# Kernel optimization log

Hardware: AMD Instinct MI355X
Metric: run time of the kernel (lower is better)

## Reference

```python
import jax, jax.numpy as jnp
import numpy as np

DIM = 1024
HEADS = 16
HEAD_DIM = DIM // HEADS
SCALE = HEAD_DIM ** -0.5


def setup_inputs() -> dict:
    key = jax.random.key(0)
    k_x, k_wqkv, k_bqkv, k_wp, k_bp = jax.random.split(key, 5)
    B, N, C = 8, 1024, DIM
    lim_qkv = 1.0 / np.sqrt(C)
    x = jax.random.normal(k_x, (B, N, C), dtype=jnp.float32)
    # store weights in [in, out] layout (torch Linear weight is [out,in]; y = x @ W.T + b)
    W_qkv = jax.random.uniform(k_wqkv, (C, 3 * C), dtype=jnp.float32, minval=-lim_qkv, maxval=lim_qkv)
    b_qkv = jax.random.uniform(k_bqkv, (3 * C,), dtype=jnp.float32, minval=-lim_qkv, maxval=lim_qkv)
    W_proj = jax.random.uniform(k_wp, (C, C), dtype=jnp.float32, minval=-lim_qkv, maxval=lim_qkv)
    b_proj = jax.random.uniform(k_bp, (C,), dtype=jnp.float32, minval=-lim_qkv, maxval=lim_qkv)
    return {"x": x, "W_qkv": W_qkv, "b_qkv": b_qkv, "W_proj": W_proj, "b_proj": b_proj}


def reference(x, W_qkv, b_qkv, W_proj, b_proj):
    B, N, C = x.shape
    H, D = HEADS, C // HEADS
    qkv = x @ W_qkv + b_qkv                          # [B, N, 3C]
    qkv = qkv.reshape(B, N, 3, H, D)
    q, k, v = jnp.moveaxis(qkv, 2, 0)                # each [B, N, H, D]
    q = q.transpose(0, 2, 1, 3)                      # [B, H, N, D]
    k = k.transpose(0, 2, 1, 3)
    v = v.transpose(0, 2, 1, 3)
    attn = jnp.einsum("bhnd,bhmd->bhnm", q, k) * SCALE
    attn = jax.nn.softmax(attn, axis=-1)
    out = jnp.einsum("bhnm,bhmd->bhnd", attn, v)     # [B, H, N, D]
    out = out.transpose(0, 2, 1, 3).reshape(B, N, C)
    return out @ W_proj + b_proj
```

## Files before the change

kernel.cpp:

```cpp
#include <hip/hip_runtime.h>
#include <hip/hip_bf16.h>


using bf16x8 = __attribute__((ext_vector_type(8))) short;
using f32x4  = __attribute__((ext_vector_type(4))) float;
using u16    = unsigned short;
using u16x8  = __attribute__((ext_vector_type(8))) unsigned short;
using u32x2  = __attribute__((ext_vector_type(2))) unsigned int;

__device__ __forceinline__ u16 f2bf(float f) {
  unsigned int u = __float_as_uint(f);
  u += 0x7FFFu + ((u >> 16) & 1u);
  return (u16)(u >> 16);
}
__device__ __forceinline__ float bf2f(u16 h) {
  return __uint_as_float(((unsigned int)h) << 16);
}
__device__ __forceinline__ unsigned cvt_pk_bf16(float a, float b) {
  unsigned r;
  asm("v_cvt_pk_bf16_f32 %0, %1, %2" : "=v"(r) : "v"(a), "v"(b));
  return r;
}
__device__ __forceinline__ float fexp2(float x) {
#if __has_builtin(__builtin_amdgcn_exp2f)
  return __builtin_amdgcn_exp2f(x);
#else
  return exp2f(x);
#endif
}

__device__ __forceinline__ void gload16(const u16* g, u16* lbase, int lane) {
#if __has_builtin(__builtin_amdgcn_global_load_lds)
  __builtin_amdgcn_global_load_lds(
      (const __attribute__((address_space(1))) void*)g,
      (__attribute__((address_space(3))) void*)lbase, 16, 0, 0);
#else
  *(u16x8*)(lbase + (size_t)lane * 8) = *(const u16x8*)g;
#endif
}

__device__ __forceinline__ void transpose_tile(
    const float* __restrict__ W, u16* __restrict__ Wt, int K, int N,
    int n0, int k0, float (*T)[65], int t)
{
  const int r = t >> 4, c4 = (t & 15) * 4;
  #pragma unroll
  for (int i = 0; i < 4; ++i) {
    f32x4 v = *(const f32x4*)&W[(size_t)(k0 + r + i * 16) * N + n0 + c4];
    T[r + i * 16][c4 + 0] = v.x;
    T[r + i * 16][c4 + 1] = v.y;
    T[r + i * 16][c4 + 2] = v.z;
    T[r + i * 16][c4 + 3] = v.w;
  }
  __syncthreads();
  const int nr = t >> 2, cs = (t & 3) * 16;
  u16x8 h0, h1;
  #pragma unroll
  for (int j = 0; j < 8; ++j) h0[j] = f2bf(T[cs + j][nr]);
  #pragma unroll
  for (int j = 0; j < 8; ++j) h1[j] = f2bf(T[cs + 8 + j][nr]);
  u16* dst = Wt + (size_t)(n0 + nr) * K + k0 + cs;
  *(u16x8*)dst = h0;
  *(u16x8*)(dst + 8) = h1;
}

__global__ __launch_bounds__(256) void prep(
    const float* __restrict__ x, u16* __restrict__ Xb,
    const float* __restrict__ Wq, u16* __restrict__ Wqt,
    const float* __restrict__ Wp, u16* __restrict__ Wpt)
{
  __shared__ float T[64][65];
  const int bid = blockIdx.x, t = threadIdx.x;
  if (bid < 4096) {
    size_t i = ((size_t)bid * 256 + t) * 8;
    f32x4 a = *(const f32x4*)(x + i);
    f32x4 b = *(const f32x4*)(x + i + 4);
    u16x8 h = { f2bf(a.x), f2bf(a.y), f2bf(a.z), f2bf(a.w),
                f2bf(b.x), f2bf(b.y), f2bf(b.z), f2bf(b.w) };
    *(u16x8*)(Xb + i) = h;
  } else if (bid < 4864) {
    const int tb = bid - 4096;
    transpose_tile(Wq, Wqt, 1024, 3072, (tb % 48) * 64, (tb / 48) * 64, T, t);
  } else {
    const int tb = bid - 4864;
    transpose_tile(Wp, Wpt, 1024, 1024, (tb % 16) * 64, (tb / 16) * 64, T, t);
  }
}

#define GEMM64_LOOP(ABASE, BBASE, AS, BS)                                     \
  const int tid = threadIdx.x;                                                \
  const int lane = tid & 63, wid = tid >> 6;                                  \
  const int wr = wid >> 1, wc = wid & 1;                                      \
  const int lg = lane >> 4, lc = lane & 15;                                   \
  const int row0 = blockIdx.x * 128, col0 = blockIdx.y * 128;                 \
  f32x4 acc[4][4];                                                            \
  _Pragma("unroll")                                                           \
  for (int m = 0; m < 4; ++m)                                                 \
    _Pragma("unroll")                                                         \
    for (int n = 0; n < 4; ++n) acc[m][n] = (f32x4){0.f, 0.f, 0.f, 0.f};      \
  const int srow = lane >> 3;                                       \
  const int sslot = (lane & 7) ^ srow;             \
  const u16* gA = (ABASE) + (size_t)(row0 + wid * 32 + srow) * 1024 + sslot * 8; \
  const u16* gB = (BBASE) + (size_t)(col0 + wid * 32 + srow) * 1024 + sslot * 8; \
  u16* lA = (AS) + wid * 2048;                                                \
  u16* lB = (BS) + wid * 2048;                                                \
  const int xr = lc & 7;                                                      \
  const int sl0 = ((0 + lg) ^ xr) * 8, sl1 = ((4 + lg) ^ xr) * 8;             \
  const int arow = (wr * 64 + lc) * 64, brow = (wc * 64 + lc) * 64;           \
  for (int k0 = 0; k0 < 1024; k0 += 64) {                                     \
    _Pragma("unroll")                                                         \
    for (int c = 0; c < 4; ++c) {                                             \
      gload16(gA + (size_t)c * 8192 + k0, lA + c * 512, lane);                \
      gload16(gB + (size_t)c * 8192 + k0, lB + c * 512, lane);                \
    }                                                                         \
    __syncthreads();                                                          \
    _Pragma("unroll")                                                         \
    for (int ks = 0; ks < 2; ++ks) {                                          \
      const int sl = ks ? sl1 : sl0;                                          \
      bf16x8 a[4], b[4];                                                      \
      _Pragma("unroll")                                                       \
      for (int m = 0; m < 4; ++m)                                             \
        a[m] = *(const bf16x8*)((AS) + arow + m * 1024 + sl);                 \
      _Pragma("unroll")                                                       \
      for (int n = 0; n < 4; ++n)                                             \
        b[n] = *(const bf16x8*)((BS) + brow + n * 1024 + sl);                 \
      __builtin_amdgcn_s_setprio(1);                                          \
      _Pragma("unroll")                                                       \
      for (int m = 0; m < 4; ++m)                                             \
        _Pragma("unroll")                                                     \
        for (int n = 0; n < 4; ++n)                                           \
          acc[m][n] = __builtin_amdgcn_mfma_f32_16x16x32_bf16(                \
              a[m], b[n], acc[m][n], 0, 0, 0);                                \
      __builtin_amdgcn_s_setprio(0);                                          \
    }                                                                         \
    __syncthreads();                                                          \
  }

__global__ __launch_bounds__(256, 2) void qkv_gemm2(
    const u16* __restrict__ Xb, const u16* __restrict__ Wt,
    const float* __restrict__ bias,
    u16* __restrict__ Qb, u16* __restrict__ Kb, u16* __restrict__ VtG)
{
  __shared__ __align__(16) u16 SM[128 * 130];
  u16* As = SM;
  u16* Bs = SM + 8192;
  u16* Tv = SM;

  GEMM64_LOOP(Xb, Wt, As, Bs)

  const int which = col0 >> 10;
  if (which == 2) {
    #pragma unroll
    for (int m = 0; m < 4; ++m) {
      #pragma unroll
      for (int n = 0; n < 4; ++n) {
        const int col = wc * 64 + n * 16 + lc;
        const float bv = bias[col0 + col];
        const int rrow = wr * 64 + m * 16 + lg * 4;
        #pragma unroll
        for (int r = 0; r < 4; ++r)
          Tv[(rrow + r) * 130 + col] = f2bf(acc[m][n][r] + bv);
      }
    }
    __syncthreads();
    const int c = tid >> 1, half = tid & 1;
    const int hh = c >> 6, d = c & 63;
    const int bb = row0 >> 10, nb = row0 & 1023;
    const int hbase = (col0 & 1023) >> 6;
    u16* vdst = VtG + ((size_t)(bb * 16 + hbase + hh) * 64 + d) * 1024
                + nb + half * 64;
    #pragma unroll
    for (int g = 0; g < 8; ++g) {
      u16x8 o;
      #pragma unroll
      for (int j = 0; j < 8; ++j)
        o[j] = Tv[(half * 64 + g * 8 + j) * 130 + c];
      *(u16x8*)(vdst + g * 8) = o;
    }
  } else {
    u16* dst = (which == 0) ? Qb : Kb;
    #pragma unroll
    for (int m = 0; m < 4; ++m) {
      #pragma unroll
      for (int n = 0; n < 4; ++n) {
        const int gc = col0 + wc * 64 + n * 16 + lc;
        const float bv = bias[gc];
        const int ci = gc & 1023, h = ci >> 6, d = ci & 63;
        const int gr0 = row0 + wr * 64 + m * 16 + lg * 4;
        const int bb = gr0 >> 10, nn0 = gr0 & 1023;
        #pragma unroll
        for (int r = 0; r < 4; ++r)
          dst[((size_t)(bb * 16 + h) * 1024 + nn0 + r) * 64 + d] =
              f2bf(acc[m][n][r] + bv);
      }
    }
  }
}

__global__ __launch_bounds__(256, 2) void attn_kernel(
    const u16* __restrict__ Q, const u16* __restrict__ K,
    const u16* __restrict__ Vt, u16* __restrict__ O)
{
  __shared__ __align__(16) u16 Ks[64 * 64];
  __shared__ __align__(16) u16 Vs[64 * 64];
  __shared__ __align__(16) u16 Pl[4 * 32 * 72];

  const int tid = threadIdx.x, lane = tid & 63, wid = tid >> 6;
  const int lg = lane >> 4, lc = lane & 15;
  const int bh = blockIdx.x;
  const int qt = blockIdx.y;
  const size_t base = (size_t)bh * 65536;
  const u16* Qp = Q + base;
  const u16* Kp = K + base;
  const u16* Vp = Vt + base;

  const float QSCALE = 0.125f * 1.44269504f;
  bf16x8 qf[2][2];
  #pragma unroll
  for (int f = 0; f < 2; ++f) {
    const u16* qsrc = Qp + (size_t)(qt * 128 + wid * 32 + f * 16 + lc) * 64 + lg * 8;
    #pragma unroll
    for (int ks = 0; ks < 2; ++ks) {
      u16x8 raw = *(const u16x8*)(qsrc + ks * 32);
      bf16x8 t;
      #pragma unroll
      for (int j = 0; j < 8; ++j) t[j] = (short)f2bf(bf2f(raw[j]) * QSCALE);
      qf[f][ks] = t;
    }
  }

  f32x4 o[2][4];
  #pragma unroll
  for (int f = 0; f < 2; ++f)
    #pragma unroll
    for (int d = 0; d < 4; ++d) o[f][d] = (f32x4){0.f, 0.f, 0.f, 0.f};
  float m_r[2] = {-1e30f, -1e30f};
  float l_r[2] = {0.f, 0.f};

  const int srow  = lane >> 3;
  const int sslot = (lane & 7) ^ srow;
  const u16* gK0 = Kp + (size_t)(wid * 16 + srow) * 64 + sslot * 8;
  const u16* gV0 = Vp + (size_t)(wid * 16 + srow) * 1024 + sslot * 8;
  u16* lK0 = Ks + wid * 1024;
  u16* lV0 = Vs + wid * 1024;

  const int xr = lc & 7;
  const int cof0 = ((0 + lg) ^ xr) * 8;
  const int cof1 = ((4 + lg) ^ xr) * 8;
  const int prow = (wid * 32 + lc) * 72;

  for (int kt = 0; kt < 16; ++kt) {
    gload16(gK0 + kt * 4096, lK0, lane);
    gload16(gK0 + kt * 4096 + 512, lK0 + 512, lane);
    gload16(gV0 + kt * 64, lV0, lane);
    gload16(gV0 + 8192 + kt * 64, lV0 + 512, lane);
    __syncthreads();

    f32x4 s[2][4];
    #pragma unroll
    for (int f = 0; f < 2; ++f)
      #pragma unroll
      for (int kb = 0; kb < 4; ++kb) s[f][kb] = (f32x4){0.f, 0.f, 0.f, 0.f};
    #pragma unroll
    for (int ks = 0; ks < 2; ++ks) {
      const int co = ks ? cof1 : cof0;
      #pragma unroll
      for (int kb = 0; kb < 4; ++kb) {
        bf16x8 kfr = *(const bf16x8*)(Ks + (kb * 16 + lc) * 64 + co);
        s[0][kb] = __builtin_amdgcn_mfma_f32_16x16x32_bf16(kfr, qf[0][ks], s[0][kb], 0, 0, 0);
        s[1][kb] = __builtin_amdgcn_mfma_f32_16x16x32_bf16(kfr, qf[1][ks], s[1][kb], 0, 0, 0);
      }
    }

    #pragma unroll
    for (int f = 0; f < 2; ++f) {
      f32x4 t01, t23;
      #pragma unroll
      for (int c = 0; c < 4; ++c) {
        t01[c] = fmaxf(s[f][0][c], s[f][1][c]);
        t23[c] = fmaxf(s[f][2][c], s[f][3][c]);
      }
      float t = fmaxf(fmaxf(fmaxf(t01[0], t01[1]), fmaxf(t01[2], t01[3])),
                      fmaxf(fmaxf(t23[0], t23[1]), fmaxf(t23[2], t23[3])));
      t = fmaxf(t, __shfl_xor(t, 16));
      t = fmaxf(t, __shfl_xor(t, 32));

      if (!__all((t - m_r[f]) <= 11.5f)) {
        float nm = fmaxf(m_r[f], t);
        float sc = fexp2(m_r[f] - nm);
        m_r[f] = nm;
        l_r[f] *= sc;
        #pragma unroll
        for (int r = 0; r < 4; ++r) {
          float scr = __shfl(sc, lg * 4 + r, 16);
          #pragma unroll
          for (int d = 0; d < 4; ++d) o[f][d][r] *= scr;
        }
      }

      float lsum = 0.f;
      #pragma unroll
      for (int kb = 0; kb < 4; ++kb) {
        f32x4 p;
        #pragma unroll
        for (int c = 0; c < 4; ++c) {
          p[c] = fexp2(s[f][kb][c] - m_r[f]);
          lsum += p[c];
        }
        u32x2 w = { cvt_pk_bf16(p[0], p[1]), cvt_pk_bf16(p[2], p[3]) };
        *(u32x2*)(Pl + prow + f * 1152 + kb * 16 + lg * 4) = w;
      }
      l_r[f] += lsum;
    }

    bf16x8 pa[2][2];
    #pragma unroll
    for (int f = 0; f < 2; ++f)
      #pragma unroll
      for (int ks = 0; ks < 2; ++ks)
        pa[f][ks] = *(const bf16x8*)(Pl + prow + f * 1152 + ks * 32 + lg * 8);
    #pragma unroll
    for (int d = 0; d < 4; ++d) {
      #pragma unroll
      for (int ks = 0; ks < 2; ++ks) {
        const int co = ks ? cof1 : cof0;
        bf16x8 vfr = *(const bf16x8*)(Vs + (d * 16 + lc) * 64 + co);
        o[0][d] = __builtin_amdgcn_mfma_f32_16x16x32_bf16(pa[0][ks], vfr, o[0][d], 0, 0, 0);
        o[1][d] = __builtin_amdgcn_mfma_f32_16x16x32_bf16(pa[1][ks], vfr, o[1][d], 0, 0, 0);
      }
    }
    __syncthreads();
  }

  const int b = bh >> 4, h = bh & 15;
  #pragma unroll
  for (int f = 0; f < 2; ++f) {
    float t = l_r[f];
    t += __shfl_xor(t, 16);
    t += __shfl_xor(t, 32);
    float linv = 1.0f / t;
    #pragma unroll
    for (int r = 0; r < 4; ++r) {
      float li = __shfl(linv, lg * 4 + r, 16);
      int n = qt * 128 + wid * 32 + f * 16 + lg * 4 + r;
      u16* dst = O + ((size_t)b * 1024 + n) * 1024 + h * 64 + lc;
      #pragma unroll
      for (int d = 0; d < 4; ++d) dst[d * 16] = f2bf(o[f][d][r] * li);
    }
  }
}

__global__ __launch_bounds__(256, 2) void proj_gemm2(
    const u16* __restrict__ Ab, const u16* __restrict__ Wt,
    const float* __restrict__ bias, float* __restrict__ Out)
{
  __shared__ __align__(16) u16 As[128 * 64];
  __shared__ __align__(16) u16 Bs[128 * 64];

  GEMM64_LOOP(Ab, Wt, As, Bs)

  #pragma unroll
  for (int m = 0; m < 4; ++m) {
    #pragma unroll
    for (int n = 0; n < 4; ++n) {
      #pragma unroll
      for (int r = 0; r < 4; ++r) {
        int gr = row0 + wr * 64 + m * 16 + lg * 4 + r;
        int gc = col0 + wc * 64 + n * 16 + lc;
        Out[(size_t)gr * 1024 + gc] = acc[m][n][r] + bias[gc];
      }
    }
  }
}

extern "C" void kernel_launch(void* const* d_in, const int* in_sizes, int n_in,
                              void* d_out, int out_size, void* d_ws, size_t ws_size,
                              hipStream_t stream) {
  const float* x     = (const float*)d_in[0];
  const float* W_qkv = (const float*)d_in[1];
  const float* b_qkv = (const float*)d_in[2];
  const float* W_prj = (const float*)d_in[3];
  const float* b_prj = (const float*)d_in[4];
  float* out = (float*)d_out;

  const size_t SEG = (size_t)8192 * 1024;
  char* ws = (char*)d_ws;
  u16* Xb  = (u16*)ws;
  u16* Ab  = Xb;
  u16* VtG = (u16*)(ws + SEG * 2);
  u16* Wqt = (u16*)(ws + SEG * 4);
  u16* Wpt = Wqt + (size_t)3072 * 1024;
  u16* Qb  = (u16*)d_out;
  u16* Kb  = Qb + SEG;

  prep<<<5120, 256, 0, stream>>>(x, Xb, W_qkv, Wqt, W_prj, Wpt);
  qkv_gemm2<<<dim3(64, 24), 256, 0, stream>>>(Xb, Wqt, b_qkv, Qb, Kb, VtG);
  attn_kernel<<<dim3(128, 8), 256, 0, stream>>>(Qb, Kb, VtG, Ab);
  proj_gemm2<<<dim3(64, 8), 256, 0, stream>>>(Ab, Wpt, b_prj, out);
}
```

Before: 150.0 us.

## Load K/V fragments directly from global into registers, drop LDS staging

The attention kernel no longer stages K and V tiles through shared memory with block-wide barriers. Each wave now loads its MFMA K and V fragments straight from global memory (relying on L1/L2 for reuse across the four waves), and the V loads are issued before the softmax so their latency overlaps it. Launch bounds are raised to allow four blocks per CU. The trade is redundant global/L2 traffic, since every wave fetches the full K/V tiles, plus higher register pressure under the tighter occupancy target, in exchange for removing the LDS round trip and the two __syncthreads per iteration.

```diff
diff --git a/kernel.cpp b/kernel.cpp
--- a/kernel.cpp
+++ b/kernel.cpp
@@ -197,12 +197,10 @@
   }
 }
 
-__global__ __launch_bounds__(256, 2) void attn_kernel(
+__global__ __launch_bounds__(256, 4) void attn_kernel(
     const u16* __restrict__ Q, const u16* __restrict__ K,
     const u16* __restrict__ Vt, u16* __restrict__ O)
 {
-  __shared__ __align__(16) u16 Ks[64 * 64];
-  __shared__ __align__(16) u16 Vs[64 * 64];
   __shared__ __align__(16) u16 Pl[4 * 32 * 72];
 
   const int tid = threadIdx.x, lane = tid & 63, wid = tid >> 6;
@@ -211,8 +209,9 @@
   const int qt = blockIdx.y;
   const size_t base = (size_t)bh * 65536;
   const u16* Qp = Q + base;
-  const u16* Kp = K + base;
-  const u16* Vp = Vt + base;
+
+  const u16* kpt = K  + base + (size_t)lc * 64 + lg * 8;
+  const u16* vpt = Vt + base + (size_t)lc * 1024 + lg * 8;
 
   const float QSCALE = 0.125f * 1.44269504f;
   bf16x8 qf[2][2];
@@ -237,24 +236,15 @@
   float m_r[2] = {-1e30f, -1e30f};
   float l_r[2] = {0.f, 0.f};
 
-  const int srow  = lane >> 3;
-  const int sslot = (lane & 7) ^ srow;
-  const u16* gK0 = Kp + (size_t)(wid * 16 + srow) * 64 + sslot * 8;
-  const u16* gV0 = Vp + (size_t)(wid * 16 + srow) * 1024 + sslot * 8;
-  u16* lK0 = Ks + wid * 1024;
-  u16* lV0 = Vs + wid * 1024;
-
-  const int xr = lc & 7;
-  const int cof0 = ((0 + lg) ^ xr) * 8;
-  const int cof1 = ((4 + lg) ^ xr) * 8;
   const int prow = (wid * 32 + lc) * 72;
 
   for (int kt = 0; kt < 16; ++kt) {
-    gload16(gK0 + kt * 4096, lK0, lane);
-    gload16(gK0 + kt * 4096 + 512, lK0 + 512, lane);
-    gload16(gV0 + kt * 64, lV0, lane);
-    gload16(gV0 + 8192 + kt * 64, lV0 + 512, lane);
-    __syncthreads();
+    bf16x8 kfr[2][4];
+    #pragma unroll
+    for (int ks = 0; ks < 2; ++ks)
+      #pragma unroll
+      for (int kb = 0; kb < 4; ++kb)
+        kfr[ks][kb] = *(const bf16x8*)(kpt + kb * 1024 + ks * 32);
 
     f32x4 s[2][4];
     #pragma unroll
@@ -263,14 +253,19 @@
       for (int kb = 0; kb < 4; ++kb) s[f][kb] = (f32x4){0.f, 0.f, 0.f, 0.f};
     #pragma unroll
     for (int ks = 0; ks < 2; ++ks) {
-      const int co = ks ? cof1 : cof0;
       #pragma unroll
       for (int kb = 0; kb < 4; ++kb) {
-        bf16x8 kfr = *(const bf16x8*)(Ks + (kb * 16 + lc) * 64 + co);
-        s[0][kb] = __builtin_amdgcn_mfma_f32_16x16x32_bf16(kfr, qf[0][ks], s[0][kb], 0, 0, 0);
-        s[1][kb] = __builtin_amdgcn_mfma_f32_16x16x32_bf16(kfr, qf[1][ks], s[1][kb], 0, 0, 0);
-      }
-    }
+        s[0][kb] = __builtin_amdgcn_mfma_f32_16x16x32_bf16(kfr[ks][kb], qf[0][ks], s[0][kb], 0, 0, 0);
+        s[1][kb] = __builtin_amdgcn_mfma_f32_16x16x32_bf16(kfr[ks][kb], qf[1][ks], s[1][kb], 0, 0, 0);
+      }
+    }
+
+    bf16x8 vfr[4][2];
+    #pragma unroll
+    for (int d = 0; d < 4; ++d)
+      #pragma unroll
+      for (int ks = 0; ks < 2; ++ks)
+        vfr[d][ks] = *(const bf16x8*)(vpt + d * 16384 + ks * 32);
 
     #pragma unroll
     for (int f = 0; f < 2; ++f) {
@@ -313,6 +308,9 @@
       l_r[f] += lsum;
     }
 
+    asm volatile("s_waitcnt lgkmcnt(0)" ::: "memory");
+    __builtin_amdgcn_sched_barrier(0);
+
     bf16x8 pa[2][2];
     #pragma unroll
     for (int f = 0; f < 2; ++f)
@@ -323,13 +321,13 @@
     for (int d = 0; d < 4; ++d) {
       #pragma unroll
       for (int ks = 0; ks < 2; ++ks) {
-        const int co = ks ? cof1 : cof0;
-        bf16x8 vfr = *(const bf16x8*)(Vs + (d * 16 + lc) * 64 + co);
-        o[0][d] = __builtin_amdgcn_mfma_f32_16x16x32_bf16(pa[0][ks], vfr, o[0][d], 0, 0, 0);
-        o[1][d] = __builtin_amdgcn_mfma_f32_16x16x32_bf16(pa[1][ks], vfr, o[1][d], 0, 0, 0);
-      }
-    }
-    __syncthreads();
+        o[0][d] = __builtin_amdgcn_mfma_f32_16x16x32_bf16(pa[0][ks], vfr[d][ks], o[0][d], 0, 0, 0);
+        o[1][d] = __builtin_amdgcn_mfma_f32_16x16x32_bf16(pa[1][ks], vfr[d][ks], o[1][d], 0, 0, 0);
+      }
+    }
+
+    kpt += 4096;
+    vpt += 64;
   }
 
   const int b = bh >> 4, h = bh & 15;
```

Result: slower. 216.6 us (+44.4%).
